# Kernel tuning notes

Hardware: AMD Instinct MI355X
Metric: run time of the kernel (lower is better)

The kernel has to match this reference:

```python
import jax, jax.numpy as jnp
import numpy as np

NUM_SUMS = 4          # num_sums: binary vectors summed per element
BVR_LEN = 16          # group length; one 16-bit word packs one bit-vector per sum
OUT_SHAPE = (8192, 8192)  # original_data_shape (64M elements, 4M groups)
NUM_GROUPS = OUT_SHAPE[0] * OUT_SHAPE[1] // BVR_LEN
CACHE_LINES = 2 ** 16  # coeff_cache has 2^16 lines per source


def setup_inputs() -> dict:
    key = jax.random.key(0)
    k1, k2, k3 = jax.random.split(key, 3)
    coeff_cache = jax.random.normal(k1, (CACHE_LINES, NUM_SUMS), dtype=jnp.float32)
    coeff_idx = jax.random.randint(k2, (NUM_GROUPS,), 0, CACHE_LINES, dtype=jnp.int32)
    # bvr: per group, NUM_SUMS packed 16-bit words (values 0..65535 carried in int32)
    bvr = jax.random.randint(k3, (NUM_GROUPS, NUM_SUMS), 0, 65536, dtype=jnp.int32)
    return {"coeff_cache": coeff_cache, "coeff_idx": coeff_idx, "bvr": bvr}


def reference(coeff_cache, coeff_idx, bvr):
    # Unpack bits: bit l of word bvr[g, s] is the selection bit of element l
    # of group g for sum s. bits: [G, S, BVR_LEN]
    shifts = jnp.arange(BVR_LEN, dtype=bvr.dtype)
    bits = ((bvr[:, :, None] >> shifts) & 1).astype(coeff_cache.dtype)
    # Per-group coefficients via codebook gather: [G, S]
    coeff = coeff_cache[coeff_idx]
    # decoded[g, l] = sum_s coeff[g, s] * bits[g, s, l]
    # (equivalent to all_points = coeff @ bin_combs.T; decoded = all_points[coeff_sel])
    decoded = jnp.einsum("gs,gsl->gl", coeff, bits)
    return decoded.reshape(OUT_SHAPE)
```

## Files before the change

### kernel.cpp

```cpp
#include <hip/hip_runtime.h>
#include <hip/hip_bf16.h>


#define NUM_SUMS 4
#define BVR_LEN 16

typedef int   i32x4 __attribute__((ext_vector_type(4)));
typedef float f32x4 __attribute__((ext_vector_type(4)));

static constexpr int THREADS_TOTAL = (8192 * 8192) / 4;
static constexpr int BLOCK = 256;

__global__ __launch_bounds__(BLOCK) void sbvr_decode_kernel(
        const float* __restrict__ coeff_cache,
        const int*   __restrict__ coeff_idx,
        const int*   __restrict__ bvr,
        float*       __restrict__ out)
{
    const int t = blockIdx.x * BLOCK + threadIdx.x;
    const int g = t >> 2;
    const int q = t & 3;

    const int   idx = __builtin_nontemporal_load(coeff_idx + g);
    const i32x4 b   = __builtin_nontemporal_load((const i32x4*)bvr + g);

    const f32x4 c = ((const f32x4*)coeff_cache)[idx];

    const int base = q * 4;
    f32x4 r;
#pragma unroll
    for (int j = 0; j < 4; ++j) {
        const int l = base + j;
        float acc = ((b.x >> l) & 1) ? c.x : 0.0f;
        acc      += ((b.y >> l) & 1) ? c.y : 0.0f;
        acc      += ((b.z >> l) & 1) ? c.z : 0.0f;
        acc      += ((b.w >> l) & 1) ? c.w : 0.0f;
        r[j] = acc;
    }
    __builtin_nontemporal_store(r, (f32x4*)out + t);
}

extern "C" void kernel_launch(void* const* d_in, const int* in_sizes, int n_in,
                              void* d_out, int out_size, void* d_ws, size_t ws_size,
                              hipStream_t stream) {
    const float* coeff_cache = (const float*)d_in[0];
    const int*   coeff_idx   = (const int*)d_in[1];
    const int*   bvr         = (const int*)d_in[2];
    float*       out         = (float*)d_out;

    const int grid = THREADS_TOTAL / BLOCK;
    sbvr_decode_kernel<<<grid, BLOCK, 0, stream>>>(coeff_cache, coeff_idx, bvr, out);
}
```

Before: 342.9 us.

## Stage group coefficients and bit-words in LDS, one load per group per block

Each block now handles 256 groups. Each thread loads one group's index, bvr words and gathered coefficients once and stores them in shared memory. After a barrier, each thread decodes four quarter-groups from LDS and writes coalesced 16-byte outputs. This removes the fourfold redundant global loads and gathers of the same group by the four threads in the old layout, at the cost of LDS traffic, a sync, and four times fewer blocks.

```diff
diff --git a/kernel.cpp b/kernel.cpp
--- a/kernel.cpp
+++ b/kernel.cpp
@@ -1,5 +1,4 @@
 #include <hip/hip_runtime.h>
-#include <hip/hip_bf16.h>
 
 
 #define NUM_SUMS 4
@@ -8,8 +7,10 @@
 typedef int   i32x4 __attribute__((ext_vector_type(4)));
 typedef float f32x4 __attribute__((ext_vector_type(4)));
 
-static constexpr int THREADS_TOTAL = (8192 * 8192) / 4;
-static constexpr int BLOCK = 256;
+static constexpr int NUM_GROUPS = (8192 * 8192) / 16;
+static constexpr int BLOCK      = 256;
+static constexpr int G_BLK      = 256;
+static constexpr int GRID       = NUM_GROUPS / G_BLK;
 
 __global__ __launch_bounds__(BLOCK) void sbvr_decode_kernel(
         const float* __restrict__ coeff_cache,
@@ -17,27 +18,42 @@
         const int*   __restrict__ bvr,
         float*       __restrict__ out)
 {
-    const int t = blockIdx.x * BLOCK + threadIdx.x;
-    const int g = t >> 2;
-    const int q = t & 3;
+    __shared__ f32x4 lds_c[G_BLK];
+    __shared__ i32x4 lds_b[G_BLK];
 
-    const int   idx = __builtin_nontemporal_load(coeff_idx + g);
-    const i32x4 b   = __builtin_nontemporal_load((const i32x4*)bvr + g);
+    const int tid = threadIdx.x;
+    const int g0  = blockIdx.x * G_BLK;
 
-    const f32x4 c = ((const f32x4*)coeff_cache)[idx];
+    {
+        const int g = g0 + tid;
+        const int   idx = __builtin_nontemporal_load(coeff_idx + g);
+        const i32x4 b   = __builtin_nontemporal_load((const i32x4*)bvr + g);
+        const f32x4 c   = ((const f32x4*)coeff_cache)[idx];
+        lds_c[tid] = c;
+        lds_b[tid] = b;
+    }
+    __syncthreads();
 
-    const int base = q * 4;
-    f32x4 r;
 #pragma unroll
-    for (int j = 0; j < 4; ++j) {
-        const int l = base + j;
-        float acc = ((b.x >> l) & 1) ? c.x : 0.0f;
-        acc      += ((b.y >> l) & 1) ? c.y : 0.0f;
-        acc      += ((b.z >> l) & 1) ? c.z : 0.0f;
-        acc      += ((b.w >> l) & 1) ? c.w : 0.0f;
-        r[j] = acc;
+    for (int p = 0; p < 4; ++p) {
+        const int gl = p * 64 + (tid >> 2);
+        const int q4 = (tid & 3) * 4;
+
+        const f32x4 c = lds_c[gl];
+        const i32x4 b = lds_b[gl];
+
+        f32x4 r;
+#pragma unroll
+        for (int j = 0; j < 4; ++j) {
+            const int l = q4 + j;
+            float acc = ((b.x >> l) & 1) ? c.x : 0.0f;
+            acc      += ((b.y >> l) & 1) ? c.y : 0.0f;
+            acc      += ((b.z >> l) & 1) ? c.z : 0.0f;
+            acc      += ((b.w >> l) & 1) ? c.w : 0.0f;
+            r[j] = acc;
+        }
+        __builtin_nontemporal_store(r, (f32x4*)out + (g0 * 4 + p * BLOCK + tid));
     }
-    __builtin_nontemporal_store(r, (f32x4*)out + t);
 }
 
 extern "C" void kernel_launch(void* const* d_in, const int* in_sizes, int n_in,
@@ -48,6 +64,5 @@
     const int*   bvr         = (const int*)d_in[2];
     float*       out         = (float*)d_out;
 
-    const int grid = THREADS_TOTAL / BLOCK;
-    sbvr_decode_kernel<<<grid, BLOCK, 0, stream>>>(coeff_cache, coeff_idx, bvr, out);
+    sbvr_decode_kernel<<<GRID, BLOCK, 0, stream>>>(coeff_cache, coeff_idx, bvr, out);
 }
```

Measured after the change: 331.5 us. 3.3% less time.
